# Performance work log

Measured on AMD Instinct MI355X. Metric: run time of the kernel, lower is better.

Reference implementation:

```python
import jax, jax.numpy as jnp
import numpy as np

N, IN_F, OUT_F = 8192, 512, 256
NEG_INF = -9e15
LEAKY_SLOPE = 0.25


def setup_inputs() -> dict:
    key = jax.random.key(0)
    k1, k2, k3, k4, k5, k6 = jax.random.split(key, 6)
    inp = {
        "input": jax.random.normal(k1, (N, IN_F), dtype=jnp.float32),
        "adj": jax.random.randint(k2, (N, N), 0, 2, dtype=jnp.int32),
        # learned params (xavier-normal-ish scale)
        "weights": jax.random.normal(k3, (IN_F, OUT_F), dtype=jnp.float32) * (2.0 / (IN_F + OUT_F)) ** 0.5,
        "a1": jax.random.normal(k4, (OUT_F, 1), dtype=jnp.float32) * (2.0 / (OUT_F + 1)) ** 0.5,
        "a2": jax.random.normal(k5, (OUT_F, 1), dtype=jnp.float32) * (2.0 / (OUT_F + 1)) ** 0.5,
        "bias": jax.random.uniform(k6, (OUT_F,), dtype=jnp.float32, minval=-1.0 / OUT_F ** 0.5, maxval=1.0 / OUT_F ** 0.5),
    }
    return inp


def reference(input, adj, weights, a1, a2, bias):
    # h = input @ W  : [N, out]
    h = input @ weights
    # e[i,j] = leaky_relu((h@a1)[i] + (h@a2)[j])  : [N, N] via broadcast
    e1 = h @ a1  # [N,1]
    e2 = h @ a2  # [N,1]
    e = e1 + e2.T
    e = jnp.where(e > 0, e, LEAKY_SLOPE * e)
    # mask non-edges, row softmax (dropout omitted: deterministic reference)
    scores = jnp.where(adj > 0, e, NEG_INF)
    attention = jax.nn.softmax(scores, axis=1)
    # aggregate + bias
    return attention @ h + bias
```

## Files before the change

kernel.cpp:

```cpp
#include <hip/hip_runtime.h>
#include <hip/hip_fp16.h>

typedef __attribute__((ext_vector_type(8))) short short8;
typedef __attribute__((ext_vector_type(4))) float floatx4;
typedef __attribute__((ext_vector_type(4))) unsigned int uintx4;
typedef __attribute__((ext_vector_type(2))) unsigned int uintx2;
typedef __attribute__((ext_vector_type(4))) int intx4;
typedef __attribute__((ext_vector_type(4))) unsigned short ushortx4;
typedef unsigned int u32;

#define NN 8192
#define KIN 512
#define COUT 256
#define SHIFT 16.0f

#define AS1 __attribute__((address_space(1)))
#define AS3 __attribute__((address_space(3)))

__device__ __forceinline__ void stage16(const void* g, void* l) {
  __builtin_amdgcn_global_load_lds((const AS1 u32*)g, (AS3 u32*)l, 16, 0, 0);
}

__device__ __forceinline__ unsigned int f2bf(float f) {
  unsigned int u = __float_as_uint(f);
  return (u + 0x7FFFu + ((u >> 16) & 1u)) >> 16;
}

__device__ __forceinline__ u32 pkbf(float lo, float hi) {
  u32 a = __float_as_uint(lo) + 0x8000u;
  u32 b = __float_as_uint(hi) + 0x8000u;
  return __builtin_amdgcn_perm(b, a, 0x07060302u);
}

__device__ __forceinline__ short8 pack8(const float* p) {
  uintx4 w;
  w.x = pkbf(p[0], p[1]);
  w.y = pkbf(p[2], p[3]);
  w.z = pkbf(p[4], p[5]);
  w.w = pkbf(p[6], p[7]);
  union { uintx4 u; short8 s; } cv; cv.u = w;
  return cv.s;
}

__global__ __launch_bounds__(256)
void k_prep(const float* __restrict__ in, ushortx4* __restrict__ inA4,
            const float* __restrict__ w, unsigned short* __restrict__ wt) {
  int b = blockIdx.x;
  if (b < 4096) {
    int idx = b * 256 + threadIdx.x;
    floatx4 v = ((const floatx4*)in)[idx];
    ushortx4 o;
    o.x = (unsigned short)f2bf(v.x);
    o.y = (unsigned short)f2bf(v.y);
    o.z = (unsigned short)f2bf(v.z);
    o.w = (unsigned short)f2bf(v.w);
    inA4[idx] = o;
  } else {
    int idx = (b - 4096) * 256 + threadIdx.x;
    int k = idx >> 8, c = idx & 255;
    wt[c * KIN + k] = (unsigned short)f2bf(w[idx]);
  }
}

__global__ __launch_bounds__(256)
void k_gemm_h(const unsigned short* __restrict__ inA, const unsigned short* __restrict__ wt,
              const float* __restrict__ a1, const float* __restrict__ a2,
              unsigned short* __restrict__ ht, float* __restrict__ e1, float* __restrict__ e2,
              float* __restrict__ A1, float* __restrict__ A2, u32* __restrict__ e2pk) {
  int wave = threadIdx.x >> 6;
  int lane = threadIdx.x & 63;
  int n = lane & 15, q = lane >> 4;
  int row0 = blockIdx.x * 64 + wave * 16;
  int mrow = row0 + n;

  floatx4 acc[16];
#pragma unroll
  for (int t = 0; t < 16; ++t) acc[t] = (floatx4){0.f, 0.f, 0.f, 0.f};

  for (int kc = 0; kc < KIN / 32; ++kc) {
    int k0 = kc * 32 + q * 8;
    short8 a = *(const short8*)(inA + (size_t)mrow * KIN + k0);
#pragma unroll
    for (int nt = 0; nt < 16; ++nt) {
      short8 b = *(const short8*)(wt + (size_t)(nt * 16 + n) * KIN + k0);
      acc[nt] = __builtin_amdgcn_mfma_f32_16x16x32_bf16(a, b, acc[nt], 0, 0, 0);
    }
  }

  int i0 = row0 + q * 4;
#pragma unroll
  for (int nt = 0; nt < 16; ++nt) {
    int c = nt * 16 + n;
    uintx2 pk;
    pk.x = f2bf(acc[nt][0]) | (f2bf(acc[nt][1]) << 16);
    pk.y = f2bf(acc[nt][2]) | (f2bf(acc[nt][3]) << 16);
    *(uintx2*)(ht + (size_t)c * NN + i0) = pk;
  }

  float s1[4] = {0.f, 0.f, 0.f, 0.f}, s2[4] = {0.f, 0.f, 0.f, 0.f};
#pragma unroll
  for (int nt = 0; nt < 16; ++nt) {
    float w1 = a1[nt * 16 + n];
    float w2 = a2[nt * 16 + n];
#pragma unroll
    for (int r = 0; r < 4; ++r) {
      s1[r] += acc[nt][r] * w1;
      s2[r] += acc[nt][r] * w2;
    }
  }
#pragma unroll
  for (int m = 1; m < 16; m <<= 1) {
#pragma unroll
    for (int r = 0; r < 4; ++r) {
      s1[r] += __shfl_xor(s1[r], m);
      s2[r] += __shfl_xor(s2[r], m);
    }
  }
  if (n == 0) {
#pragma unroll
    for (int r = 0; r < 4; ++r) {
      float v1 = s1[r], v2 = s2[r];
      e1[i0 + r] = v1;
      e2[i0 + r] = v2;
      A1[i0 + r] = __expf(v1 - 8.0f);
      A2[i0 + r] = __expf(0.25f * v1 - 8.0f);
      u32 b1 = f2bf(__expf(v2 - 8.0f));
      u32 b2 = f2bf(__expf(0.25f * v2 - 8.0f));
      e2pk[i0 + r] = (b1 << 16) | b2;
    }
  }
}

__global__ __launch_bounds__(256, 2)
void k_attn_v3(const int* __restrict__ adj, const unsigned short* __restrict__ ht,
               const float* __restrict__ A1, const float* __restrict__ A2,
               const u32* __restrict__ e2pk,
               __half2* __restrict__ oph, float* __restrict__ Dpart) {
  __shared__ __align__(16) char smem[36864];
  u32* e2s = (u32*)(smem + 32768);

  int b = blockIdx.x;
  int rg = b >> 3, js = b & 7;
  int wave = threadIdx.x >> 6, lane = threadIdx.x & 63;
  int n = lane & 15, q = lane >> 4;
  int rowbase = rg * 128 + wave * 32;
  int jbeg = js * 1024;
  int swz = q ^ ((n >> 1) & 3);

  float A1v0 = A1[rowbase + n],      A2v0 = A2[rowbase + n];
  float A1v1 = A1[rowbase + 16 + n], A2v1 = A2[rowbase + 16 + n];

  floatx4 acc[2][16];
  floatx4 accd[2];
#pragma unroll
  for (int t = 0; t < 2; ++t) {
    accd[t] = (floatx4){0.f, 0.f, 0.f, 0.f};
#pragma unroll
    for (int nt = 0; nt < 16; ++nt) acc[t][nt] = (floatx4){0.f, 0.f, 0.f, 0.f};
  }

  union { uintx4 u; short8 s; } onesu;
  onesu.u = (uintx4){0x3F803F80u, 0x3F803F80u, 0x3F803F80u, 0x3F803F80u};
  short8 ones = onesu.s;

  const int* ar0 = adj + (size_t)(rowbase + n) * NN + jbeg + q * 8;
  const int* ar1 = adj + (size_t)(rowbase + 16 + n) * NN + jbeg + q * 8;

  auto stage = [&](int ch, int buf) {
    int j0g = jbeg + ch * 32;
    char* hbase = smem + buf * 16384;
#pragma unroll
    for (int i = 0; i < 4; ++i) {
      int seg = wave * 256 + i * 64 + lane;
      int c = seg >> 2;
      int o = (seg & 3) ^ ((seg >> 3) & 3);
      stage16(ht + (size_t)c * NN + j0g + o * 8, hbase + (size_t)(wave * 256 + i * 64) * 16);
    }
  };

  intx4 aA[4], aB[4];

  stage(0, 0);
  aA[0] = *(const intx4*)(ar0);
  aA[1] = *(const intx4*)(ar0 + 4);
  aA[2] = *(const intx4*)(ar1);
  aA[3] = *(const intx4*)(ar1 + 4);
  ((uintx4*)e2s)[threadIdx.x] = *(const uintx4*)(e2pk + jbeg + threadIdx.x * 4);
  asm volatile("s_waitcnt lgkmcnt(0)" ::: "memory");
  asm volatile("s_barrier" ::: "memory");

  auto body = [&](int ch, intx4* aC, intx4* aN) {
    int cur = ch & 1;
    if (ch < 31) {
      stage(ch + 1, cur ^ 1);
      int jn = (ch + 1) * 32;
      aN[0] = *(const intx4*)(ar0 + jn);
      aN[1] = *(const intx4*)(ar0 + jn + 4);
      aN[2] = *(const intx4*)(ar1 + jn);
      aN[3] = *(const intx4*)(ar1 + jn + 4);
    }

    uintx4 ba = *(const uintx4*)(e2s + ch * 32 + q * 8);
    uintx4 bb = *(const uintx4*)(e2s + ch * 32 + q * 8 + 4);
    u32 bw[8] = {ba.x, ba.y, ba.z, ba.w, bb.x, bb.y, bb.z, bb.w};

    float p0[8], p1[8];
#pragma unroll
    for (int jj = 0; jj < 8; ++jj) {
      int av0 = (jj < 4) ? aC[0][jj] : aC[1][jj - 4];
      int av1 = (jj < 4) ? aC[2][jj] : aC[3][jj - 4];
      float B1 = __uint_as_float(bw[jj] & 0xffff0000u);
      float B2 = __uint_as_float(bw[jj] << 16);
      float m10 = A1v0 * B1, m20 = A2v0 * B2;
      float m11 = A1v1 * B1, m21 = A2v1 * B2;
      float pm0 = fmaxf(m10, m20);
      float pm1 = fmaxf(m11, m21);
      p0[jj] = (av0 != 0) ? pm0 : 0.f;
      p1[jj] = (av1 != 0) ? pm1 : 0.f;
    }
    short8 af0 = pack8(p0);
    short8 af1 = pack8(p1);

    if (ch < 31) {
      asm volatile("s_waitcnt vmcnt(8)" ::: "memory");
    } else {
      asm volatile("s_waitcnt vmcnt(0)" ::: "memory");
    }
    asm volatile("s_barrier" ::: "memory");

    const short8* lb = (const short8*)(smem + (size_t)cur * 16384);
#pragma unroll
    for (int t = 0; t < 16; ++t) {
      short8 bfv = lb[t * 64 + n * 4 + swz];
      acc[0][t] = __builtin_amdgcn_mfma_f32_16x16x32_bf16(af0, bfv, acc[0][t], 0, 0, 0);
      acc[1][t] = __builtin_amdgcn_mfma_f32_16x16x32_bf16(af1, bfv, acc[1][t], 0, 0, 0);
    }
    accd[0] = __builtin_amdgcn_mfma_f32_16x16x32_bf16(af0, ones, accd[0], 0, 0, 0);
    accd[1] = __builtin_amdgcn_mfma_f32_16x16x32_bf16(af1, ones, accd[1], 0, 0, 0);

    asm volatile("s_waitcnt lgkmcnt(0)" ::: "memory");
    asm volatile("s_barrier" ::: "memory");
  };

  for (int ch = 0; ch < 32; ch += 2) {
    body(ch, aA, aB);
    body(ch + 1, aB, aA);
  }

  if (n == 0) {
#pragma unroll
    for (int t2 = 0; t2 < 2; ++t2)
#pragma unroll
      for (int r = 0; r < 4; ++r)
        Dpart[(size_t)js * NN + rowbase + t2 * 16 + q * 4 + r] = accd[t2][r];
  }

#pragma unroll
  for (int t2 = 0; t2 < 2; ++t2) {
    int ibase = rowbase + t2 * 16 + q * 4;
#pragma unroll
    for (int nt = 0; nt < 16; ++nt) {
      int c = nt * 16 + n;
      oph[((size_t)js * 4096 + (ibase >> 1)) * 256 + c] =
          __floats2half2_rn(acc[t2][nt][0], acc[t2][nt][1]);
      oph[((size_t)js * 4096 + (ibase >> 1) + 1) * 256 + c] =
          __floats2half2_rn(acc[t2][nt][2], acc[t2][nt][3]);
    }
  }
}

__global__ void k_final_part(float* __restrict__ out, const __half2* __restrict__ oph,
                             const float* __restrict__ Dpart, const float* __restrict__ bias) {
  int i = blockIdx.x;
  int c = threadIdx.x;
  int hi = i & 1;
  float s = 0.f, d = 0.f;
#pragma unroll
  for (int js = 0; js < 8; ++js) {
    __half2 h2 = oph[((size_t)js * 4096 + (i >> 1)) * 256 + c];
    s += hi ? __high2float(h2) : __low2float(h2);
    d += Dpart[(size_t)js * NN + i];
  }
  out[(size_t)i * COUT + c] = s / fmaxf(d, 1e-37f) + bias[c];
}

__global__ __launch_bounds__(256, 2)
void k_attn_atomic(const int* __restrict__ adj, const unsigned short* __restrict__ ht,
                   const float* __restrict__ e1, const float* __restrict__ e2,
                   float* __restrict__ out_num, float* __restrict__ Dbuf) {
  int b = blockIdx.x;
  int rg = b >> 3, js = b & 7;
  int wave = threadIdx.x >> 6, lane = threadIdx.x & 63;
  int n = lane & 15, q = lane >> 4;
  int rowbase = rg * 128 + wave * 32;

  float e1v0 = e1[rowbase + n];
  float e1v1 = e1[rowbase + 16 + n];

  floatx4 acc[2][16];
#pragma unroll
  for (int t = 0; t < 2; ++t)
#pragma unroll
    for (int nt = 0; nt < 16; ++nt) acc[t][nt] = (floatx4){0.f, 0.f, 0.f, 0.f};

  float d0 = 0.f, d1 = 0.f;
  int jbeg = js * 1024;

  for (int ch = 0; ch < 32; ++ch) {
    int j0 = jbeg + ch * 32 + q * 8;
    floatx4 ea = *(const floatx4*)(e2 + j0);
    floatx4 eb = *(const floatx4*)(e2 + j0 + 4);
    float ev[8] = {ea.x, ea.y, ea.z, ea.w, eb.x, eb.y, eb.z, eb.w};

    intx4 A00 = *(const intx4*)(adj + (size_t)(rowbase + n) * NN + j0);
    intx4 A01 = *(const intx4*)(adj + (size_t)(rowbase + n) * NN + j0 + 4);
    intx4 A10 = *(const intx4*)(adj + (size_t)(rowbase + 16 + n) * NN + j0);
    intx4 A11 = *(const intx4*)(adj + (size_t)(rowbase + 16 + n) * NN + j0 + 4);

    float p0[8], p1[8];
#pragma unroll
    for (int jj = 0; jj < 8; ++jj) {
      int av0 = (jj < 4) ? A00[jj] : A01[jj - 4];
      int av1 = (jj < 4) ? A10[jj] : A11[jj - 4];
      float t0 = e1v0 + ev[jj];
      float t1 = e1v1 + ev[jj];
      float f0 = fmaxf(t0, 0.25f * t0);
      float f1 = fmaxf(t1, 0.25f * t1);
      float x0 = __expf(f0 - SHIFT);
      float x1 = __expf(f1 - SHIFT);
      p0[jj] = (av0 != 0) ? x0 : 0.f;
      p1[jj] = (av1 != 0) ? x1 : 0.f;
      d0 += p0[jj];
      d1 += p1[jj];
    }
    short8 af0 = pack8(p0);
    short8 af1 = pack8(p1);

#pragma unroll
    for (int g = 0; g < 2; ++g) {
      short8 bf[8];
#pragma unroll
      for (int t = 0; t < 8; ++t)
        bf[t] = *(const short8*)(ht + (size_t)((g * 8 + t) * 16 + n) * NN + j0);
#pragma unroll
      for (int t = 0; t < 8; ++t) {
        acc[0][g * 8 + t] = __builtin_amdgcn_mfma_f32_16x16x32_bf16(af0, bf[t], acc[0][g * 8 + t], 0, 0, 0);
        acc[1][g * 8 + t] = __builtin_amdgcn_mfma_f32_16x16x32_bf16(af1, bf[t], acc[1][g * 8 + t], 0, 0, 0);
      }
    }
  }

  d0 += __shfl_xor(d0, 16); d0 += __shfl_xor(d0, 32);
  d1 += __shfl_xor(d1, 16); d1 += __shfl_xor(d1, 32);
  if (lane < 16) {
    atomicAdd(Dbuf + rowbase + lane, d0);
    atomicAdd(Dbuf + rowbase + 16 + lane, d1);
  }

#pragma unroll
  for (int t2 = 0; t2 < 2; ++t2) {
#pragma unroll
    for (int nt = 0; nt < 16; ++nt) {
#pragma unroll
      for (int r = 0; r < 4; ++r) {
        int i = rowbase + t2 * 16 + q * 4 + r;
        atomicAdd(out_num + (size_t)i * COUT + nt * 16 + n, acc[t2][nt][r]);
      }
    }
  }
}

__global__ void k_final_atomic(float* __restrict__ out, const float* __restrict__ Dbuf,
                               const float* __restrict__ bias) {
  int idx = blockIdx.x * 256 + threadIdx.x;
  int i = idx >> 8, c = idx & 255;
  float d = fmaxf(Dbuf[i], 1e-37f);
  out[idx] = out[idx] / d + bias[c];
}

extern "C" void kernel_launch(void* const* d_in, const int* in_sizes, int n_in,
                              void* d_out, int out_size, void* d_ws, size_t ws_size,
                              hipStream_t stream) {
  const float* input   = (const float*)d_in[0];
  const int*   adj     = (const int*)d_in[1];
  const float* weights = (const float*)d_in[2];
  const float* a1      = (const float*)d_in[3];
  const float* a2      = (const float*)d_in[4];
  const float* bias    = (const float*)d_in[5];
  float* out = (float*)d_out;
  char* ws = (char*)d_ws;

  unsigned short* inA = (unsigned short*)(ws);
  unsigned short* wt  = (unsigned short*)(ws + 8388608);
  unsigned short* ht  = (unsigned short*)(ws + 8650752);
  float* e1    = (float*)(ws + 12845056);
  float* e2    = (float*)(ws + 12877824);
  float* A1    = (float*)(ws + 12910592);
  float* A2    = (float*)(ws + 12943360);
  u32*   e2pk  = (u32*)  (ws + 12976128);
  float* Dpart = (float*)(ws + 13008896);
  __half2* oph = (__half2*)(ws + 13271040);
  const size_t WS_NEEDED_PART = 13271040 + (size_t)8 * NN * COUT * 2;
  float* Dbuf = Dpart;

  k_prep<<<4608, 256, 0, stream>>>(input, (ushortx4*)inA, weights, wt);
  k_gemm_h<<<128, 256, 0, stream>>>(inA, wt, a1, a2, ht, e1, e2, A1, A2, e2pk);

  if (ws_size >= WS_NEEDED_PART) {
    k_attn_v3<<<512, 256, 0, stream>>>(adj, ht, A1, A2, e2pk, oph, Dpart);
    k_final_part<<<8192, 256, 0, stream>>>(out, oph, Dpart, bias);
  } else {
    hipMemsetAsync(out, 0, (size_t)NN * COUT * sizeof(float), stream);
    hipMemsetAsync(Dbuf, 0, NN * sizeof(float), stream);
    k_attn_atomic<<<512, 256, 0, stream>>>(adj, ht, e1, e2, out, Dbuf);
    k_final_atomic<<<8192, 256, 0, stream>>>(out, Dbuf, bias);
  }
}
```

Baseline: 454.4 us.

## Deepen attention pipeline to four LDS buffers with prefetch distance two

```diff
diff --git a/kernel.cpp b/kernel.cpp
--- a/kernel.cpp
+++ b/kernel.cpp
@@ -62,7 +62,7 @@
   }
 }
 
-__global__ __launch_bounds__(256)
+__global__ __launch_bounds__(128)
 void k_gemm_h(const unsigned short* __restrict__ inA, const unsigned short* __restrict__ wt,
               const float* __restrict__ a1, const float* __restrict__ a2,
               unsigned short* __restrict__ ht, float* __restrict__ e1, float* __restrict__ e2,
@@ -70,7 +70,7 @@
   int wave = threadIdx.x >> 6;
   int lane = threadIdx.x & 63;
   int n = lane & 15, q = lane >> 4;
-  int row0 = blockIdx.x * 64 + wave * 16;
+  int row0 = blockIdx.x * 32 + wave * 16;
   int mrow = row0 + n;
 
   floatx4 acc[16];
@@ -132,12 +132,12 @@
 }
 
 __global__ __launch_bounds__(256, 2)
-void k_attn_v3(const int* __restrict__ adj, const unsigned short* __restrict__ ht,
+void k_attn_v4(const int* __restrict__ adj, const unsigned short* __restrict__ ht,
                const float* __restrict__ A1, const float* __restrict__ A2,
                const u32* __restrict__ e2pk,
                __half2* __restrict__ oph, float* __restrict__ Dpart) {
-  __shared__ __align__(16) char smem[36864];
-  u32* e2s = (u32*)(smem + 32768);
+  __shared__ __align__(16) char smem[69632];
+  u32* e2s = (u32*)(smem + 65536);
 
   int b = blockIdx.x;
   int rg = b >> 3, js = b & 7;
@@ -178,27 +178,27 @@
     }
   };
 
-  intx4 aA[4], aB[4];
-
+  intx4 aE[4], aO[4];
+
+  ((uintx4*)e2s)[threadIdx.x] = *(const uintx4*)(e2pk + jbeg + threadIdx.x * 4);
+  asm volatile("" ::: "memory");
   stage(0, 0);
-  aA[0] = *(const intx4*)(ar0);
-  aA[1] = *(const intx4*)(ar0 + 4);
-  aA[2] = *(const intx4*)(ar1);
-  aA[3] = *(const intx4*)(ar1 + 4);
-  ((uintx4*)e2s)[threadIdx.x] = *(const uintx4*)(e2pk + jbeg + threadIdx.x * 4);
+  aE[0] = *(const intx4*)(ar0);
+  aE[1] = *(const intx4*)(ar0 + 4);
+  aE[2] = *(const intx4*)(ar1);
+  aE[3] = *(const intx4*)(ar1 + 4);
+  asm volatile("" ::: "memory");
+  stage(1, 1);
+  aO[0] = *(const intx4*)(ar0 + 32);
+  aO[1] = *(const intx4*)(ar0 + 36);
+  aO[2] = *(const intx4*)(ar1 + 32);
+  aO[3] = *(const intx4*)(ar1 + 36);
   asm volatile("s_waitcnt lgkmcnt(0)" ::: "memory");
   asm volatile("s_barrier" ::: "memory");
 
-  auto body = [&](int ch, intx4* aC, intx4* aN) {
-    int cur = ch & 1;
-    if (ch < 31) {
-      stage(ch + 1, cur ^ 1);
-      int jn = (ch + 1) * 32;
-      aN[0] = *(const intx4*)(ar0 + jn);
-      aN[1] = *(const intx4*)(ar0 + jn + 4);
-      aN[2] = *(const intx4*)(ar1 + jn);
-      aN[3] = *(const intx4*)(ar1 + jn + 4);
-    }
+  auto body = [&](int ch, intx4* aC, int mode) {
+    int buf = ch & 3;
+    if (mode == 0) stage(ch + 2, (ch + 2) & 3);
 
     uintx4 ba = *(const uintx4*)(e2s + ch * 32 + q * 8);
     uintx4 bb = *(const uintx4*)(e2s + ch * 32 + q * 8 + 4);
@@ -221,14 +221,20 @@
     short8 af0 = pack8(p0);
     short8 af1 = pack8(p1);
 
-    if (ch < 31) {
-      asm volatile("s_waitcnt vmcnt(8)" ::: "memory");
-    } else {
-      asm volatile("s_waitcnt vmcnt(0)" ::: "memory");
-    }
+    if (mode == 0) {
+      int jn = (ch + 2) * 32;
+      aC[0] = *(const intx4*)(ar0 + jn);
+      aC[1] = *(const intx4*)(ar0 + jn + 4);
+      aC[2] = *(const intx4*)(ar1 + jn);
+      aC[3] = *(const intx4*)(ar1 + jn + 4);
+    }
+
+    if (mode == 0)      asm volatile("s_waitcnt vmcnt(16)" ::: "memory");
+    else if (mode == 1) asm volatile("s_waitcnt vmcnt(8)" ::: "memory");
+    else                asm volatile("s_waitcnt vmcnt(0)" ::: "memory");
     asm volatile("s_barrier" ::: "memory");
 
-    const short8* lb = (const short8*)(smem + (size_t)cur * 16384);
+    const short8* lb = (const short8*)(smem + (size_t)buf * 16384);
 #pragma unroll
     for (int t = 0; t < 16; ++t) {
       short8 bfv = lb[t * 64 + n * 4 + swz];
@@ -237,15 +243,14 @@
     }
     accd[0] = __builtin_amdgcn_mfma_f32_16x16x32_bf16(af0, ones, accd[0], 0, 0, 0);
     accd[1] = __builtin_amdgcn_mfma_f32_16x16x32_bf16(af1, ones, accd[1], 0, 0, 0);
-
-    asm volatile("s_waitcnt lgkmcnt(0)" ::: "memory");
-    asm volatile("s_barrier" ::: "memory");
   };
 
-  for (int ch = 0; ch < 32; ch += 2) {
-    body(ch, aA, aB);
-    body(ch + 1, aB, aA);
-  }
+  for (int ch = 0; ch < 30; ch += 2) {
+    body(ch, aE, 0);
+    body(ch + 1, aO, 0);
+  }
+  body(30, aE, 1);
+  body(31, aO, 2);
 
   if (n == 0) {
 #pragma unroll
@@ -404,10 +409,10 @@
   float* Dbuf = Dpart;
 
   k_prep<<<4608, 256, 0, stream>>>(input, (ushortx4*)inA, weights, wt);
-  k_gemm_h<<<128, 256, 0, stream>>>(inA, wt, a1, a2, ht, e1, e2, A1, A2, e2pk);
+  k_gemm_h<<<256, 128, 0, stream>>>(inA, wt, a1, a2, ht, e1, e2, A1, A2, e2pk);
 
   if (ws_size >= WS_NEEDED_PART) {
-    k_attn_v3<<<512, 256, 0, stream>>>(adj, ht, A1, A2, e2pk, oph, Dpart);
+    k_attn_v4<<<512, 256, 0, stream>>>(adj, ht, A1, A2, e2pk, oph, Dpart);
     k_final_part<<<8192, 256, 0, stream>>>(out, oph, Dpart, bias);
   } else {
     hipMemsetAsync(out, 0, (size_t)NN * COUT * sizeof(float), stream);
```

Measured after the change: 446.0 us. Within noise of the previous version (-1.8%).

## Fuse input bf16 conversion into GEMM and double attention column splits

Applied to the files above, without the earlier changes.

```diff
diff --git a/kernel.cpp b/kernel.cpp
--- a/kernel.cpp
+++ b/kernel.cpp
@@ -6,7 +6,6 @@
 typedef __attribute__((ext_vector_type(4))) unsigned int uintx4;
 typedef __attribute__((ext_vector_type(2))) unsigned int uintx2;
 typedef __attribute__((ext_vector_type(4))) int intx4;
-typedef __attribute__((ext_vector_type(4))) unsigned short ushortx4;
 typedef unsigned int u32;
 
 #define NN 8192
@@ -43,34 +42,21 @@
 }
 
 __global__ __launch_bounds__(256)
-void k_prep(const float* __restrict__ in, ushortx4* __restrict__ inA4,
-            const float* __restrict__ w, unsigned short* __restrict__ wt) {
-  int b = blockIdx.x;
-  if (b < 4096) {
-    int idx = b * 256 + threadIdx.x;
-    floatx4 v = ((const floatx4*)in)[idx];
-    ushortx4 o;
-    o.x = (unsigned short)f2bf(v.x);
-    o.y = (unsigned short)f2bf(v.y);
-    o.z = (unsigned short)f2bf(v.z);
-    o.w = (unsigned short)f2bf(v.w);
-    inA4[idx] = o;
-  } else {
-    int idx = (b - 4096) * 256 + threadIdx.x;
-    int k = idx >> 8, c = idx & 255;
-    wt[c * KIN + k] = (unsigned short)f2bf(w[idx]);
-  }
-}
-
-__global__ __launch_bounds__(256)
-void k_gemm_h(const unsigned short* __restrict__ inA, const unsigned short* __restrict__ wt,
+void k_prep_w(const float* __restrict__ w, unsigned short* __restrict__ wt) {
+  int idx = blockIdx.x * 256 + threadIdx.x;
+  int k = idx >> 8, c = idx & 255;
+  wt[c * KIN + k] = (unsigned short)f2bf(w[idx]);
+}
+
+__global__ __launch_bounds__(128)
+void k_gemm_h(const float* __restrict__ input, const unsigned short* __restrict__ wt,
               const float* __restrict__ a1, const float* __restrict__ a2,
               unsigned short* __restrict__ ht, float* __restrict__ e1, float* __restrict__ e2,
               float* __restrict__ A1, float* __restrict__ A2, u32* __restrict__ e2pk) {
   int wave = threadIdx.x >> 6;
   int lane = threadIdx.x & 63;
   int n = lane & 15, q = lane >> 4;
-  int row0 = blockIdx.x * 64 + wave * 16;
+  int row0 = blockIdx.x * 32 + wave * 16;
   int mrow = row0 + n;
 
   floatx4 acc[16];
@@ -79,7 +65,15 @@
 
   for (int kc = 0; kc < KIN / 32; ++kc) {
     int k0 = kc * 32 + q * 8;
-    short8 a = *(const short8*)(inA + (size_t)mrow * KIN + k0);
+    floatx4 av0 = *(const floatx4*)(input + (size_t)mrow * KIN + k0);
+    floatx4 av1 = *(const floatx4*)(input + (size_t)mrow * KIN + k0 + 4);
+    uintx4 aw;
+    aw.x = f2bf(av0.x) | (f2bf(av0.y) << 16);
+    aw.y = f2bf(av0.z) | (f2bf(av0.w) << 16);
+    aw.z = f2bf(av1.x) | (f2bf(av1.y) << 16);
+    aw.w = f2bf(av1.z) | (f2bf(av1.w) << 16);
+    union { uintx4 u; short8 s; } acv; acv.u = aw;
+    short8 a = acv.s;
 #pragma unroll
     for (int nt = 0; nt < 16; ++nt) {
       short8 b = *(const short8*)(wt + (size_t)(nt * 16 + n) * KIN + k0);
@@ -132,19 +126,19 @@
 }
 
 __global__ __launch_bounds__(256, 2)
-void k_attn_v3(const int* __restrict__ adj, const unsigned short* __restrict__ ht,
+void k_attn_v5(const int* __restrict__ adj, const unsigned short* __restrict__ ht,
                const float* __restrict__ A1, const float* __restrict__ A2,
                const u32* __restrict__ e2pk,
                __half2* __restrict__ oph, float* __restrict__ Dpart) {
-  __shared__ __align__(16) char smem[36864];
+  __shared__ __align__(16) char smem[34816];
   u32* e2s = (u32*)(smem + 32768);
 
   int b = blockIdx.x;
-  int rg = b >> 3, js = b & 7;
+  int rg = b >> 4, js = b & 15;
   int wave = threadIdx.x >> 6, lane = threadIdx.x & 63;
   int n = lane & 15, q = lane >> 4;
   int rowbase = rg * 128 + wave * 32;
-  int jbeg = js * 1024;
+  int jbeg = js * 512;
   int swz = q ^ ((n >> 1) & 3);
 
   float A1v0 = A1[rowbase + n],      A2v0 = A2[rowbase + n];
@@ -180,18 +174,20 @@
 
   intx4 aA[4], aB[4];
 
+  uintx2 ev = *(const uintx2*)(e2pk + jbeg + threadIdx.x * 2);
+  asm volatile("" ::: "memory");
   stage(0, 0);
   aA[0] = *(const intx4*)(ar0);
   aA[1] = *(const intx4*)(ar0 + 4);
   aA[2] = *(const intx4*)(ar1);
   aA[3] = *(const intx4*)(ar1 + 4);
-  ((uintx4*)e2s)[threadIdx.x] = *(const uintx4*)(e2pk + jbeg + threadIdx.x * 4);
+  ((uintx2*)e2s)[threadIdx.x] = ev;
   asm volatile("s_waitcnt lgkmcnt(0)" ::: "memory");
   asm volatile("s_barrier" ::: "memory");
 
   auto body = [&](int ch, intx4* aC, intx4* aN) {
     int cur = ch & 1;
-    if (ch < 31) {
+    if (ch < 15) {
       stage(ch + 1, cur ^ 1);
       int jn = (ch + 1) * 32;
       aN[0] = *(const intx4*)(ar0 + jn);
@@ -221,7 +217,7 @@
     short8 af0 = pack8(p0);
     short8 af1 = pack8(p1);
 
-    if (ch < 31) {
+    if (ch < 15) {
       asm volatile("s_waitcnt vmcnt(8)" ::: "memory");
     } else {
       asm volatile("s_waitcnt vmcnt(0)" ::: "memory");
@@ -242,7 +238,7 @@
     asm volatile("s_barrier" ::: "memory");
   };
 
-  for (int ch = 0; ch < 32; ch += 2) {
+  for (int ch = 0; ch < 16; ch += 2) {
     body(ch, aA, aB);
     body(ch + 1, aB, aA);
   }
@@ -276,7 +272,7 @@
   int hi = i & 1;
   float s = 0.f, d = 0.f;
 #pragma unroll
-  for (int js = 0; js < 8; ++js) {
+  for (int js = 0; js < 16; ++js) {
     __half2 h2 = oph[((size_t)js * 4096 + (i >> 1)) * 256 + c];
     s += hi ? __high2float(h2) : __low2float(h2);
     d += Dpart[(size_t)js * NN + i];
@@ -390,24 +386,23 @@
   float* out = (float*)d_out;
   char* ws = (char*)d_ws;
 
-  unsigned short* inA = (unsigned short*)(ws);
-  unsigned short* wt  = (unsigned short*)(ws + 8388608);
-  unsigned short* ht  = (unsigned short*)(ws + 8650752);
-  float* e1    = (float*)(ws + 12845056);
-  float* e2    = (float*)(ws + 12877824);
-  float* A1    = (float*)(ws + 12910592);
-  float* A2    = (float*)(ws + 12943360);
-  u32*   e2pk  = (u32*)  (ws + 12976128);
-  float* Dpart = (float*)(ws + 13008896);
-  __half2* oph = (__half2*)(ws + 13271040);
-  const size_t WS_NEEDED_PART = 13271040 + (size_t)8 * NN * COUT * 2;
+  unsigned short* ht  = (unsigned short*)(ws);
+  unsigned short* wt  = (unsigned short*)(ws + 4194304);
+  float* e1    = (float*)(ws + 4456448);
+  float* e2    = (float*)(ws + 4489216);
+  float* A1    = (float*)(ws + 4521984);
+  float* A2    = (float*)(ws + 4554752);
+  u32*   e2pk  = (u32*)  (ws + 4587520);
+  float* Dpart = (float*)(ws + 4620288);
+  __half2* oph = (__half2*)(ws + 5144576);
+  const size_t WS_NEEDED_PART = 5144576 + (size_t)16 * NN * COUT * 2;
   float* Dbuf = Dpart;
 
-  k_prep<<<4608, 256, 0, stream>>>(input, (ushortx4*)inA, weights, wt);
-  k_gemm_h<<<128, 256, 0, stream>>>(inA, wt, a1, a2, ht, e1, e2, A1, A2, e2pk);
+  k_prep_w<<<512, 256, 0, stream>>>(weights, wt);
+  k_gemm_h<<<256, 128, 0, stream>>>(input, wt, a1, a2, ht, e1, e2, A1, A2, e2pk);
 
   if (ws_size >= WS_NEEDED_PART) {
-    k_attn_v3<<<512, 256, 0, stream>>>(adj, ht, A1, A2, e2pk, oph, Dpart);
+    k_attn_v5<<<1024, 256, 0, stream>>>(adj, ht, A1, A2, e2pk, oph, Dpart);
     k_final_part<<<8192, 256, 0, stream>>>(out, oph, Dpart, bias);
   } else {
     hipMemsetAsync(out, 0, (size_t)NN * COUT * sizeof(float), stream);
```

Result: slower. 478.9 us (+5.4%).
